# Optimization experiments

Measured on AMD Instinct MI355X. Metric: run time of the kernel, lower is better.

The kernel has to match this reference:

```python
import jax, jax.numpy as jnp
import numpy as np

D_MODEL = 2048
N_HEADS = 16
N_KV_HEADS = 4
HEAD_DIM = 128
ROPE_THETA = 10000.0


def _rope_cos_sin(T, hd, theta):
    # [T, hd//2]
    inv_freq = 1.0 / (theta ** (jnp.arange(0, hd, 2, dtype=jnp.float32) / hd))
    ang = jnp.arange(T, dtype=jnp.float32)[:, None] * inv_freq[None, :]
    return jnp.cos(ang), jnp.sin(ang)


def _apply_rope(x, cos, sin):
    # x: [B, H, T, hd]; rotate-half (Llama-style) RoPE
    hd = x.shape[-1]
    x1, x2 = x[..., : hd // 2], x[..., hd // 2 :]
    c = cos[None, None, :, :]
    s = sin[None, None, :, :]
    return jnp.concatenate([x1 * c - x2 * s, x2 * c + x1 * s], axis=-1)


def setup_inputs() -> dict:
    key = jax.random.key(0)
    ks = jax.random.split(key, 5)
    B, T = 2, 2048
    x = jax.random.normal(ks[0], (B, T, D_MODEL), dtype=jnp.float32)
    sq = 1.0 / np.sqrt(D_MODEL)
    Wq = jax.random.normal(ks[1], (D_MODEL, N_HEADS * HEAD_DIM), dtype=jnp.float32) * sq
    Wk = jax.random.normal(ks[2], (D_MODEL, N_KV_HEADS * HEAD_DIM), dtype=jnp.float32) * sq
    Wv = jax.random.normal(ks[3], (D_MODEL, N_KV_HEADS * HEAD_DIM), dtype=jnp.float32) * sq
    Wo = jax.random.normal(ks[4], (N_HEADS * HEAD_DIM, D_MODEL), dtype=jnp.float32) * sq
    return {"x": x, "Wq": Wq, "Wk": Wk, "Wv": Wv, "Wo": Wo}


def reference(x, Wq, Wk, Wv, Wo):
    B, T, _ = x.shape
    H, KV, hd = N_HEADS, N_KV_HEADS, HEAD_DIM
    n_rep = H // KV

    q = (x @ Wq).reshape(B, T, H, hd).transpose(0, 2, 1, 3)    # [B,H,T,hd]
    k = (x @ Wk).reshape(B, T, KV, hd).transpose(0, 2, 1, 3)   # [B,KV,T,hd]
    v = (x @ Wv).reshape(B, T, KV, hd).transpose(0, 2, 1, 3)

    cos, sin = _rope_cos_sin(T, hd, ROPE_THETA)
    q = _apply_rope(q, cos, sin)
    k = _apply_rope(k, cos, sin)

    # repeat KV heads for GQA: [B,KV,T,hd] -> [B,H,T,hd]
    k = jnp.repeat(k, n_rep, axis=1)
    v = jnp.repeat(v, n_rep, axis=1)

    scale = 1.0 / jnp.sqrt(jnp.float32(hd))
    scores = jnp.einsum("bhqd,bhkd->bhqk", q, k) * scale       # [B,H,T,T]
    causal = jnp.tril(jnp.ones((T, T), dtype=bool))
    scores = jnp.where(causal[None, None, :, :], scores, -jnp.inf)
    attn = jax.nn.softmax(scores, axis=-1)
    out = jnp.einsum("bhqk,bhkd->bhqd", attn, v)               # [B,H,T,hd]
    out = out.transpose(0, 2, 1, 3).reshape(B, T, H * hd)
    return out @ Wo
```

## Files before the change

### kernel.cpp

```cpp
#include <hip/hip_runtime.h>
#include <stdint.h>

#define T_SEQ 2048
#define DM    2048
#define NH    16
#define NKV   4
#define HD    128
#define MROWS 4096
#define NQKV  3072

typedef unsigned short u16;
typedef __bf16 bf16x8 __attribute__((ext_vector_type(8)));
typedef float  f32x4  __attribute__((ext_vector_type(4)));

__device__ __forceinline__ u16 f2b(float f) {
  union { float f; unsigned u; } v; v.f = f;
  return (u16)((v.u + 0x7fffu + ((v.u >> 16) & 1u)) >> 16);
}
__device__ __forceinline__ float b2f(u16 u) {
  union { unsigned u; float f; } v; v.u = ((unsigned)u) << 16;
  return v.f;
}
__device__ __forceinline__ void gl_lds16(const u16* g, u16* l) {
  __builtin_amdgcn_global_load_lds(
      (__attribute__((address_space(1))) void*)g,
      (__attribute__((address_space(3))) void*)l, 16, 0, 0);
}
__device__ __forceinline__ void storev(float* p, float v) { *p = v; }
__device__ __forceinline__ void storev(u16* p, float v)   { *p = f2b(v); }

__global__ __launch_bounds__(256) void k_cvt_x(const float* __restrict__ x,
                                               u16* __restrict__ o, int n) {
  int i = (blockIdx.x * 256 + threadIdx.x) * 4;
  if (i >= n) return;
  float4 v = *(const float4*)(x + i);
  ushort4 r;
  r.x = f2b(v.x); r.y = f2b(v.y); r.z = f2b(v.z); r.w = f2b(v.w);
  *(ushort4*)(o + i) = r;
}

__global__ __launch_bounds__(256) void k_tw4(const float* __restrict__ Wq,
                                             const float* __restrict__ Wk,
                                             const float* __restrict__ Wv,
                                             const float* __restrict__ Wo,
                                             u16* __restrict__ WT,
                                             u16* __restrict__ Wot) {
  __shared__ float tl[32][33];
  int z = blockIdx.z;
  const float* in; u16* out; int Nd, xt;
  if (z < 64)      { in = Wq; out = WT;               Nd = 2048; xt = z; }
  else if (z < 80) { in = Wk; out = WT + 2048 * 2048; Nd = 512;  xt = z - 64; }
  else if (z < 96) { in = Wv; out = WT + 2560 * 2048; Nd = 512;  xt = z - 80; }
  else             { in = Wo; out = Wot;              Nd = 2048; xt = z - 96; }
  int n0 = xt * 32, k0 = blockIdx.y * 32;
  int tx = threadIdx.x, ty = threadIdx.y;
#pragma unroll
  for (int i = 0; i < 32; i += 8)
    tl[ty + i][tx] = in[(long)(k0 + ty + i) * Nd + n0 + tx];
  __syncthreads();
#pragma unroll
  for (int i = 0; i < 32; i += 8)
    out[(long)(n0 + ty + i) * 2048 + k0 + tx] = f2b(tl[tx][ty + i]);
}

template <typename OutT>
__global__ __launch_bounds__(256) void k_gemm(const u16* __restrict__ A,
                                              const u16* __restrict__ Bt,
                                              OutT* __restrict__ C,
                                              int M, int N, int K) {
  __shared__ __align__(16) u16 As[128 * 32];
  __shared__ __align__(16) u16 Bs[128 * 32];
  const int tid = threadIdx.x;
  const int wv = tid >> 6, lane = tid & 63;
  const int quad = lane >> 4, ln = lane & 15;
  const int wm = wv & 1, wn = wv >> 1;
  const int rchnk = quad ^ ((ln >> 1) & 3);
  const long m0 = (long)blockIdx.x * 128;
  const long n0 = (long)blockIdx.y * 128;
  f32x4 acc[4][4] = {};
  for (int k0 = 0; k0 < K; k0 += 32) {
#pragma unroll
    for (int r = 0; r < 2; ++r) {
      int c = r * 256 + tid;
      int gc = (c & 3) ^ ((c >> 3) & 3);
      gl_lds16(A  + (m0 + (c >> 2)) * K + k0 + gc * 8, &As[(r * 256 + wv * 64) * 8]);
      gl_lds16(Bt + (n0 + (c >> 2)) * K + k0 + gc * 8, &Bs[(r * 256 + wv * 64) * 8]);
    }
    __syncthreads();
    bf16x8 af[4], bg[4];
#pragma unroll
    for (int i = 0; i < 4; ++i)
      af[i] = *(const bf16x8*)&As[(wm * 64 + i * 16 + ln) * 32 + rchnk * 8];
#pragma unroll
    for (int j = 0; j < 4; ++j)
      bg[j] = *(const bf16x8*)&Bs[(wn * 64 + j * 16 + ln) * 32 + rchnk * 8];
#pragma unroll
    for (int i = 0; i < 4; ++i)
#pragma unroll
      for (int j = 0; j < 4; ++j)
        acc[i][j] = __builtin_amdgcn_mfma_f32_16x16x32_bf16(af[i], bg[j], acc[i][j], 0, 0, 0);
    __syncthreads();
  }
#pragma unroll
  for (int i = 0; i < 4; ++i) {
    long row = m0 + wm * 64 + i * 16 + quad * 4;
#pragma unroll
    for (int j = 0; j < 4; ++j) {
      long col = n0 + wn * 64 + j * 16 + ln;
#pragma unroll
      for (int r = 0; r < 4; ++r)
        storev(&C[(row + r) * N + col], acc[i][j][r]);
    }
  }
}

__global__ __launch_bounds__(256) void k_rope2(const u16* __restrict__ C,
                                               u16* __restrict__ Qo,
                                               u16* __restrict__ Ko) {
  int idx = blockIdx.x * 256 + threadIdx.x;
  int d = idx & 63;
  int t = (idx >> 6) & (T_SEQ - 1);
  int g = idx >> 17;
  int b = (g >= 20) ? 1 : 0;
  int hh = g - b * 20;
  int isQ = hh < 16;
  int head = isQ ? hh : (hh - 16);
  int coloff = isQ ? 0 : 2048;
  float qscale = isQ ? 0.12751745f : 1.0f;
  u16* o = isQ ? Qo : Ko;
  int nh = isQ ? NH : NKV;
  long inb = (long)(b * T_SEQ + t) * NQKV + coloff + head * HD + d;
  float q1 = b2f(C[inb]);
  float q2 = b2f(C[inb + 64]);
  float inv = __expf(-0.14391156f * (float)d);
  float sn, cs;
  __sincosf((float)t * inv, &sn, &cs);
  long ob = (((long)b * nh + head) * T_SEQ + t) * HD + d;
  o[ob]      = f2b((q1 * cs - q2 * sn) * qscale);
  o[ob + 64] = f2b((q2 * cs + q1 * sn) * qscale);
}

__global__ __launch_bounds__(256) void k_vt(const u16* __restrict__ C,
                                            u16* __restrict__ Vt) {
  __shared__ u16 tl[32][33];
  int bkv = blockIdx.z;
  int t0 = blockIdx.x * 32, d0 = blockIdx.y * 32;
  int tx = threadIdx.x, ty = threadIdx.y;
  int b = bkv >> 2, kv = bkv & 3;
#pragma unroll
  for (int i = 0; i < 32; i += 8)
    tl[ty + i][tx] = C[(long)(b * T_SEQ + t0 + ty + i) * NQKV + 2560 + kv * HD + d0 + tx];
  __syncthreads();
#pragma unroll
  for (int i = 0; i < 32; i += 8)
    Vt[((long)bkv * HD + d0 + ty + i) * T_SEQ + t0 + tx] = tl[tx][ty + i];
}

template <bool DIAG>
__device__ __forceinline__ void p_emit(f32x4 (&S)[4], u16* __restrict__ Pb,
                                       int quad, int ln, int mrow) {
#pragma unroll
  for (int nt = 0; nt < 4; ++nt)
#pragma unroll
    for (int r = 0; r < 4; ++r) {
      float v = S[nt][r];
      if (DIAG) v = (nt * 16 + ln <= mrow + r) ? v : -1e30f;
      float pv = exp2f(v - 8.0f);
      int row = quad * 4 + r;
      int chnk = (nt * 2 + (ln >> 3)) ^ (row & 7);
      *(__bf16*)&Pb[row * 64 + chnk * 8 + (ln & 7)] = (__bf16)pv;
    }
}

__global__ __launch_bounds__(256, 2) void k_attn(const u16* __restrict__ Q,
                                                 const u16* __restrict__ Kg,
                                                 const u16* __restrict__ Vt,
                                                 u16* __restrict__ Og) {
  __shared__ __align__(16) u16 Ks[64 * 128];
  __shared__ __align__(16) u16 Vs[128 * 64];
  __shared__ __align__(16) u16 Ps[4][2][16 * 64];
  const int tid = threadIdx.x;
  const int wv = tid >> 6, lane = tid & 63;
  const int quad = lane >> 4, ln = lane & 15;
  const int bh = blockIdx.y;
  const int b = bh >> 4, h = bh & 15;
  const int kvh = h >> 2;
  const int p = blockIdx.x;
  const int thi = 31 - p, tlo = p;
  const int qhi = thi * 64 + wv * 16;
  const int qlo = tlo * 64 + wv * 16;

  bf16x8 qfh[4], qfl[4];
  {
    const u16* qp = Q + ((long)bh * T_SEQ + qhi + ln) * HD + quad * 8;
#pragma unroll
    for (int s = 0; s < 4; ++s) qfh[s] = *(const bf16x8*)(qp + s * 32);
    qp = Q + ((long)bh * T_SEQ + qlo + ln) * HD + quad * 8;
#pragma unroll
    for (int s = 0; s < 4; ++s) qfl[s] = *(const bf16x8*)(qp + s * 32);
  }
  bf16x8 onesb;
#pragma unroll
  for (int i = 0; i < 8; ++i) onesb[i] = (__bf16)1.0f;

  f32x4 lh = {0.f, 0.f, 0.f, 0.f}, ll = {0.f, 0.f, 0.f, 0.f};
  f32x4 oh[8] = {}, ol[8] = {};

  const u16* Kb = Kg + (long)(b * NKV + kvh) * T_SEQ * HD;
  const u16* Vb = Vt + (long)(b * NKV + kvh) * HD * T_SEQ;

  for (int kt = 0; kt <= thi; ++kt) {
    const int k0 = kt * 64;
#pragma unroll
    for (int r = 0; r < 4; ++r) {
      int s = r * 256 + tid;
      gl_lds16(Kb + (long)(k0 + (s >> 4)) * HD + (((s & 15) ^ ((s >> 4) & 15)) << 3),
               &Ks[(r * 256 + wv * 64) * 8]);
      gl_lds16(Vb + (long)(s >> 3) * T_SEQ + k0 + (((s & 7) ^ ((s >> 3) & 7)) << 3),
               &Vs[(r * 256 + wv * 64) * 8]);
    }
    __syncthreads();
    const bool lo_act = (kt <= tlo);
    f32x4 Sh[4], Sl[4];
#pragma unroll
    for (int nt = 0; nt < 4; ++nt) {
      bf16x8 kb[4];
      const u16* kp = &Ks[(nt * 16 + ln) * 128];
#pragma unroll
      for (int ss = 0; ss < 4; ++ss)
        kb[ss] = *(const bf16x8*)(kp + (((quad + 4 * ss) ^ ln) << 3));
      f32x4 s = {0.f, 0.f, 0.f, 0.f};
#pragma unroll
      for (int ss = 0; ss < 4; ++ss)
        s = __builtin_amdgcn_mfma_f32_16x16x32_bf16(qfh[ss], kb[ss], s, 0, 0, 0);
      Sh[nt] = s;
      if (lo_act) {
        f32x4 t = {0.f, 0.f, 0.f, 0.f};
#pragma unroll
        for (int ss = 0; ss < 4; ++ss)
          t = __builtin_amdgcn_mfma_f32_16x16x32_bf16(qfl[ss], kb[ss], t, 0, 0, 0);
        Sl[nt] = t;
      }
    }
    if (kt == thi) p_emit<true>(Sh, &Ps[wv][0][0], quad, ln, wv * 16 + quad * 4);
    else           p_emit<false>(Sh, &Ps[wv][0][0], quad, ln, 0);
    if (lo_act) {
      if (kt == tlo) p_emit<true>(Sl, &Ps[wv][1][0], quad, ln, wv * 16 + quad * 4);
      else           p_emit<false>(Sl, &Ps[wv][1][0], quad, ln, 0);
    }
    asm volatile("s_waitcnt lgkmcnt(0)" ::: "memory");
    bf16x8 pfh[2], pfl[2];
#pragma unroll
    for (int ss = 0; ss < 2; ++ss)
      pfh[ss] = *(const bf16x8*)&Ps[wv][0][ln * 64 + (((ss * 4 + quad) ^ (ln & 7)) << 3)];
    if (lo_act) {
#pragma unroll
      for (int ss = 0; ss < 2; ++ss)
        pfl[ss] = *(const bf16x8*)&Ps[wv][1][ln * 64 + (((ss * 4 + quad) ^ (ln & 7)) << 3)];
    }
    lh = __builtin_amdgcn_mfma_f32_16x16x32_bf16(pfh[0], onesb, lh, 0, 0, 0);
    lh = __builtin_amdgcn_mfma_f32_16x16x32_bf16(pfh[1], onesb, lh, 0, 0, 0);
    if (lo_act) {
      ll = __builtin_amdgcn_mfma_f32_16x16x32_bf16(pfl[0], onesb, ll, 0, 0, 0);
      ll = __builtin_amdgcn_mfma_f32_16x16x32_bf16(pfl[1], onesb, ll, 0, 0, 0);
    }
#pragma unroll
    for (int dt = 0; dt < 8; ++dt) {
      bf16x8 vb[2];
      const u16* vp = &Vs[(dt * 16 + ln) * 64];
#pragma unroll
      for (int ss = 0; ss < 2; ++ss)
        vb[ss] = *(const bf16x8*)(vp + (((quad + 4 * ss) ^ (ln & 7)) << 3));
#pragma unroll
      for (int ss = 0; ss < 2; ++ss)
        oh[dt] = __builtin_amdgcn_mfma_f32_16x16x32_bf16(pfh[ss], vb[ss], oh[dt], 0, 0, 0);
      if (lo_act) {
#pragma unroll
        for (int ss = 0; ss < 2; ++ss)
          ol[dt] = __builtin_amdgcn_mfma_f32_16x16x32_bf16(pfl[ss], vb[ss], ol[dt], 0, 0, 0);
      }
    }
    __syncthreads();
  }
  float rh[4], rl[4];
#pragma unroll
  for (int r = 0; r < 4; ++r) { rh[r] = 1.f / lh[r]; rl[r] = 1.f / ll[r]; }
#pragma unroll
  for (int dt = 0; dt < 8; ++dt)
#pragma unroll
    for (int r = 0; r < 4; ++r) {
      long rowh = (long)b * T_SEQ + qhi + quad * 4 + r;
      long rowl = (long)b * T_SEQ + qlo + quad * 4 + r;
      Og[rowh * (NH * HD) + h * HD + dt * 16 + ln] = f2b(oh[dt][r] * rh[r]);
      Og[rowl * (NH * HD) + h * HD + dt * 16 + ln] = f2b(ol[dt][r] * rl[r]);
    }
}

extern "C" void kernel_launch(void* const* d_in, const int* in_sizes, int n_in,
                              void* d_out, int out_size, void* d_ws, size_t ws_size,
                              hipStream_t stream) {
  const float* x  = (const float*)d_in[0];
  const float* Wq = (const float*)d_in[1];
  const float* Wk = (const float*)d_in[2];
  const float* Wv = (const float*)d_in[3];
  const float* Wo = (const float*)d_in[4];
  float* out = (float*)d_out;
  char* ws = (char*)d_ws;
  u16* WT  = (u16*)(ws + 0);
  u16* Wot = (u16*)(ws + 12582912);
  u16* Cq  = (u16*)(ws + 20971520);
  u16* Xb  = (u16*)(ws + 46137344);
  u16* Kb  = (u16*)(ws + 62914560);
  u16* Vtb = (u16*)(ws + 67108864);
  u16* Qb = Xb;
  u16* attn = Cq;

  k_cvt_x<<<8192, 256, 0, stream>>>(x, Xb, MROWS * DM);
  k_tw4<<<dim3(1, 64, 160), dim3(32, 8), 0, stream>>>(Wq, Wk, Wv, Wo, WT, Wot);

  k_gemm<u16><<<dim3(32, 24), 256, 0, stream>>>(Xb, WT, Cq, MROWS, NQKV, DM);

  k_rope2<<<20480, 256, 0, stream>>>(Cq, Qb, Kb);
  k_vt<<<dim3(64, 4, 8), dim3(32, 8), 0, stream>>>(Cq, Vtb);

  k_attn<<<dim3(16, 32), 256, 0, stream>>>(Qb, Kb, Vtb, attn);

  k_gemm<float><<<dim3(32, 16), 256, 0, stream>>>(attn, Wot, out, MROWS, DM, 2048);
}
```

Measured before the change: 312.5 us.

## Fuse RoPE and V transpose into QKV GEMM epilogue

The QKV projection GEMM now writes its outputs directly in the attention layouts. Q/K tiles are staged through shared memory and get RoPE and scaling applied before vectorized stores, and V tiles are stored transposed. This drops the intermediate QKV buffer round trip and two extra kernel launches (rope and V transpose). In exchange the GEMM epilogue is longer, with extra syncs and scattered strided V stores.

```diff
diff --git a/kernel.cpp b/kernel.cpp
--- a/kernel.cpp
+++ b/kernel.cpp
@@ -12,6 +12,7 @@
 typedef unsigned short u16;
 typedef __bf16 bf16x8 __attribute__((ext_vector_type(8)));
 typedef float  f32x4  __attribute__((ext_vector_type(4)));
+typedef u16    u16x8  __attribute__((ext_vector_type(8)));
 
 __device__ __forceinline__ u16 f2b(float f) {
   union { float f; unsigned u; } v; v.f = f;
@@ -61,6 +62,107 @@
 #pragma unroll
   for (int i = 0; i < 32; i += 8)
     out[(long)(n0 + ty + i) * 2048 + k0 + tx] = f2b(tl[tx][ty + i]);
+}
+
+__global__ __launch_bounds__(256) void k_gemm_qkv(const u16* __restrict__ A,
+                                                  const u16* __restrict__ Bt,
+                                                  u16* __restrict__ Qo,
+                                                  u16* __restrict__ Ko,
+                                                  u16* __restrict__ Vo) {
+  __shared__ __align__(16) u16 smem[64 * 136];
+  u16* As = smem;
+  u16* Bs = smem + 4096;
+  const int tid = threadIdx.x;
+  const int wv = tid >> 6, lane = tid & 63;
+  const int quad = lane >> 4, ln = lane & 15;
+  const int wm = wv & 1, wn = wv >> 1;
+  const int rchnk = quad ^ ((ln >> 1) & 3);
+  const int m0i = blockIdx.x * 128;
+  const int by = blockIdx.y;
+  const long m0 = m0i, n0 = (long)by * 128;
+  f32x4 acc[4][4] = {};
+  for (int k0 = 0; k0 < DM; k0 += 32) {
+#pragma unroll
+    for (int r = 0; r < 2; ++r) {
+      int c = r * 256 + tid;
+      int gc = (c & 3) ^ ((c >> 3) & 3);
+      gl_lds16(A  + (m0 + (c >> 2)) * DM + k0 + gc * 8, &As[(r * 256 + wv * 64) * 8]);
+      gl_lds16(Bt + (n0 + (c >> 2)) * DM + k0 + gc * 8, &Bs[(r * 256 + wv * 64) * 8]);
+    }
+    __syncthreads();
+    bf16x8 af[4], bg[4];
+#pragma unroll
+    for (int i = 0; i < 4; ++i)
+      af[i] = *(const bf16x8*)&As[(wm * 64 + i * 16 + ln) * 32 + rchnk * 8];
+#pragma unroll
+    for (int j = 0; j < 4; ++j)
+      bg[j] = *(const bf16x8*)&Bs[(wn * 64 + j * 16 + ln) * 32 + rchnk * 8];
+#pragma unroll
+    for (int i = 0; i < 4; ++i)
+#pragma unroll
+      for (int j = 0; j < 4; ++j)
+        acc[i][j] = __builtin_amdgcn_mfma_f32_16x16x32_bf16(af[i], bg[j], acc[i][j], 0, 0, 0);
+    __syncthreads();
+  }
+  if (by < 20) {
+    const bool isQ = by < 16;
+    const int head = isQ ? by : by - 16;
+    const int nh = isQ ? NH : NKV;
+    const float qs = isQ ? 0.12751745f : 1.0f;
+    u16* dst = isQ ? Qo : Ko;
+#pragma unroll
+    for (int r0 = 0; r0 < 128; r0 += 64) {
+      if (wm == (r0 >> 6)) {
+#pragma unroll
+        for (int i = 0; i < 4; ++i)
+#pragma unroll
+          for (int j = 0; j < 4; ++j)
+#pragma unroll
+            for (int r = 0; r < 4; ++r)
+              smem[(i * 16 + quad * 4 + r) * 136 + wn * 64 + j * 16 + ln] =
+                  f2b(acc[i][j][r]);
+      }
+      __syncthreads();
+      int row = tid >> 2, dc = (tid & 3) * 16;
+      int t = m0i + r0 + row;
+      int t2 = t & (T_SEQ - 1), bb = t >> 11;
+      const u16* cr = &smem[row * 136];
+      long ob = ((long)(bb * nh + head) * T_SEQ + t2) * HD;
+      u16x8 oA[2], oB[2];
+#pragma unroll
+      for (int g = 0; g < 2; ++g)
+#pragma unroll
+        for (int dd = 0; dd < 8; ++dd) {
+          int d = dc + g * 8 + dd;
+          float c1 = b2f(cr[d]), c2 = b2f(cr[d + 64]);
+          float inv = __expf(-0.14391156f * (float)d);
+          float sn, cn;
+          __sincosf((float)t2 * inv, &sn, &cn);
+          oA[g][dd] = f2b((c1 * cn - c2 * sn) * qs);
+          oB[g][dd] = f2b((c2 * cn + c1 * sn) * qs);
+        }
+      *(u16x8*)&dst[ob + dc]          = oA[0];
+      *(u16x8*)&dst[ob + dc + 8]      = oA[1];
+      *(u16x8*)&dst[ob + 64 + dc]     = oB[0];
+      *(u16x8*)&dst[ob + 64 + dc + 8] = oB[1];
+      __syncthreads();
+    }
+  } else {
+    const int kv = by - 20;
+    const int bb = m0i >> 11, t0i = m0i & (T_SEQ - 1);
+#pragma unroll
+    for (int i = 0; i < 4; ++i)
+#pragma unroll
+      for (int j = 0; j < 4; ++j) {
+        int d = wn * 64 + j * 16 + ln;
+        int t = t0i + wm * 64 + i * 16 + quad * 4;
+        long vo = ((long)((bb * NKV + kv) * HD) + d) * T_SEQ + t;
+        ushort4 pk;
+        pk.x = f2b(acc[i][j][0]); pk.y = f2b(acc[i][j][1]);
+        pk.z = f2b(acc[i][j][2]); pk.w = f2b(acc[i][j][3]);
+        *(ushort4*)&Vo[vo] = pk;
+      }
+  }
 }
 
 template <typename OutT>
@@ -112,48 +214,6 @@
         storev(&C[(row + r) * N + col], acc[i][j][r]);
     }
   }
-}
-
-__global__ __launch_bounds__(256) void k_rope2(const u16* __restrict__ C,
-                                               u16* __restrict__ Qo,
-                                               u16* __restrict__ Ko) {
-  int idx = blockIdx.x * 256 + threadIdx.x;
-  int d = idx & 63;
-  int t = (idx >> 6) & (T_SEQ - 1);
-  int g = idx >> 17;
-  int b = (g >= 20) ? 1 : 0;
-  int hh = g - b * 20;
-  int isQ = hh < 16;
-  int head = isQ ? hh : (hh - 16);
-  int coloff = isQ ? 0 : 2048;
-  float qscale = isQ ? 0.12751745f : 1.0f;
-  u16* o = isQ ? Qo : Ko;
-  int nh = isQ ? NH : NKV;
-  long inb = (long)(b * T_SEQ + t) * NQKV + coloff + head * HD + d;
-  float q1 = b2f(C[inb]);
-  float q2 = b2f(C[inb + 64]);
-  float inv = __expf(-0.14391156f * (float)d);
-  float sn, cs;
-  __sincosf((float)t * inv, &sn, &cs);
-  long ob = (((long)b * nh + head) * T_SEQ + t) * HD + d;
-  o[ob]      = f2b((q1 * cs - q2 * sn) * qscale);
-  o[ob + 64] = f2b((q2 * cs + q1 * sn) * qscale);
-}
-
-__global__ __launch_bounds__(256) void k_vt(const u16* __restrict__ C,
-                                            u16* __restrict__ Vt) {
-  __shared__ u16 tl[32][33];
-  int bkv = blockIdx.z;
-  int t0 = blockIdx.x * 32, d0 = blockIdx.y * 32;
-  int tx = threadIdx.x, ty = threadIdx.y;
-  int b = bkv >> 2, kv = bkv & 3;
-#pragma unroll
-  for (int i = 0; i < 32; i += 8)
-    tl[ty + i][tx] = C[(long)(b * T_SEQ + t0 + ty + i) * NQKV + 2560 + kv * HD + d0 + tx];
-  __syncthreads();
-#pragma unroll
-  for (int i = 0; i < 32; i += 8)
-    Vt[((long)bkv * HD + d0 + ty + i) * T_SEQ + t0 + tx] = tl[tx][ty + i];
 }
 
 template <bool DIAG>
@@ -308,20 +368,16 @@
   char* ws = (char*)d_ws;
   u16* WT  = (u16*)(ws + 0);
   u16* Wot = (u16*)(ws + 12582912);
-  u16* Cq  = (u16*)(ws + 20971520);
-  u16* Xb  = (u16*)(ws + 46137344);
-  u16* Kb  = (u16*)(ws + 62914560);
-  u16* Vtb = (u16*)(ws + 67108864);
-  u16* Qb = Xb;
-  u16* attn = Cq;
+  u16* Xb  = (u16*)(ws + 20971520);
+  u16* Qb  = (u16*)(ws + 37748736);
+  u16* Kb  = (u16*)(ws + 54525952);
+  u16* Vtb = (u16*)(ws + 58720256);
+  u16* attn = Xb;
 
   k_cvt_x<<<8192, 256, 0, stream>>>(x, Xb, MROWS * DM);
   k_tw4<<<dim3(1, 64, 160), dim3(32, 8), 0, stream>>>(Wq, Wk, Wv, Wo, WT, Wot);
 
-  k_gemm<u16><<<dim3(32, 24), 256, 0, stream>>>(Xb, WT, Cq, MROWS, NQKV, DM);
-
-  k_rope2<<<20480, 256, 0, stream>>>(Cq, Qb, Kb);
-  k_vt<<<dim3(64, 4, 8), dim3(32, 8), 0, stream>>>(Cq, Vtb);
+  k_gemm_qkv<<<dim3(32, 24), 256, 0, stream>>>(Xb, WT, Qb, Kb, Vtb);
 
   k_attn<<<dim3(16, 32), 256, 0, stream>>>(Qb, Kb, Vtb, attn);
 
```

After: 351.2 us. 12.4% more time.
